# Optimization experiments

Hardware: AMD Instinct MI355X
Metric: run time of the kernel (lower is better)

The kernel has to match this reference:

```python
import jax, jax.numpy as jnp
from jax import lax
import numpy as np

N_HEAD = 16
KERNEL = 3
ROPE_BASE = 10000.0


def _rope_tables(T, D, dtype):
    inv_freq = 1.0 / (ROPE_BASE ** (jnp.arange(0, D, 2, dtype=jnp.float32) / D))
    t = jnp.arange(T, dtype=jnp.float32)
    freqs = t[:, None] * inv_freq[None, :]           # [T, D/2]
    emb = jnp.concatenate([freqs, freqs], axis=-1)   # [T, D]
    return jnp.cos(emb).astype(dtype), jnp.sin(emb).astype(dtype)


def _rotate_half(x):
    x1, x2 = jnp.split(x, 2, axis=-1)
    return jnp.concatenate([-x2, x1], axis=-1)


def setup_inputs() -> dict:
    key = jax.random.key(0)
    k1, k2, k3, k4 = jax.random.split(key, 4)
    B, T, C = 2, 2048, 2048
    s = 0.02
    return {
        "x": jax.random.normal(k1, (B, T, C), dtype=jnp.float32),
        "conv_w": jax.random.normal(k2, (C, 1, KERNEL), dtype=jnp.float32) * s,
        "w_attn": jax.random.normal(k3, (3 * C, C), dtype=jnp.float32) * s,
        "w_proj": jax.random.normal(k4, (C, C), dtype=jnp.float32) * s,
    }


def reference(x, conv_w, w_attn, w_proj):
    B, T, C = x.shape
    H = N_HEAD
    D = C // H

    # causal depthwise conv1d: left-pad K-1, groups=C
    xc = jnp.transpose(x, (0, 2, 1))                       # [B, C, T]
    xc = jnp.pad(xc, ((0, 0), (0, 0), (KERNEL - 1, 0)))
    xc = lax.conv_general_dilated(
        xc, conv_w, window_strides=(1,), padding="VALID",
        feature_group_count=C, dimension_numbers=("NCH", "OIH", "NCH"))
    xconv = jnp.transpose(xc, (0, 2, 1))                   # [B, T, C]

    # fused QKV projection
    qkv = xconv @ w_attn.T                                 # [B, T, 3C]
    q, k, v = jnp.split(qkv, 3, axis=-1)
    q = q.reshape(B, T, H, D)
    k = k.reshape(B, T, H, D)
    v = v.reshape(B, T, H, D)

    # rotary embedding
    cos, sin = _rope_tables(T, D, x.dtype)                 # [T, D]
    cos = cos[None, :, None, :]
    sin = sin[None, :, None, :]
    q = q * cos + _rotate_half(q) * sin
    k = k * cos + _rotate_half(k) * sin

    # causal SDPA
    scale = 1.0 / jnp.sqrt(jnp.asarray(D, dtype=x.dtype))
    scores = jnp.einsum("bthd,bshd->bhts", q, k) * scale   # [B, H, T, T]
    causal = jnp.tril(jnp.ones((T, T), dtype=bool))
    scores = jnp.where(causal[None, None], scores, jnp.finfo(scores.dtype).min)
    p = jax.nn.softmax(scores, axis=-1)
    y = jnp.einsum("bhts,bshd->bthd", p, v).reshape(B, T, C)

    return y @ w_proj.T
```

## Files before the change

kernel.cpp:

```cpp
#include <hip/hip_runtime.h>

typedef __attribute__((ext_vector_type(8))) short bf16x8;
typedef __attribute__((ext_vector_type(4))) float f32x4;
typedef __attribute__((ext_vector_type(4))) unsigned short u16x4;

#define DEV static __device__ __forceinline__

DEV float bf2f(unsigned short u) {
  union { unsigned int i; float f; } v; v.i = ((unsigned int)u) << 16; return v.f;
}
DEV unsigned short f2bf(float f) {
  unsigned int x = __float_as_uint(f);
  x += 0x7fffu + ((x >> 16) & 1u);
  return (unsigned short)(x >> 16);
}
DEV f32x4 mfma16(bf16x8 a, bf16x8 b, f32x4 c) {
  return __builtin_amdgcn_mfma_f32_16x16x32_bf16(a, b, c, 0, 0, 0);
}
DEV void gload_lds16(const void* g, void* l) {
  __builtin_amdgcn_global_load_lds(
      (const __attribute__((address_space(1))) unsigned int*)g,
      (__attribute__((address_space(3))) unsigned int*)l, 16, 0, 0);
}

__global__ void build_tables(float* __restrict__ ct, float* __restrict__ st) {
  int idx = blockIdx.x * 256 + threadIdx.x;
  int i = idx & 63, t = idx >> 6;
  float f = powf(10000.0f, -(float)i * (1.0f / 64.0f));
  float a = (float)t * f;
  ct[idx] = cosf(a);
  st[idx] = sinf(a);
}

__global__ void cast_bf(const float* __restrict__ in, unsigned short* __restrict__ out, int n4) {
  int idx = blockIdx.x * 256 + threadIdx.x;
  if (idx >= n4) return;
  f32x4 v = *(const f32x4*)(in + (size_t)idx * 4);
  u16x4 o;
  #pragma unroll
  for (int j = 0; j < 4; ++j) o[j] = f2bf(v[j]);
  *(u16x4*)(out + (size_t)idx * 4) = o;
}

__global__ void conv_cast(const float* __restrict__ x, const float* __restrict__ w,
                          unsigned short* __restrict__ out) {
  int idx = blockIdx.x * 256 + threadIdx.x;
  int c4 = idx & 511, t = (idx >> 9) & 2047;
  int c = c4 * 4;
  const float* xp = x + (size_t)(idx >> 20) * 2048 * 2048 + (size_t)t * 2048 + c;
  f32x4 v2 = *(const f32x4*)xp;
  f32x4 v1 = {0.f, 0.f, 0.f, 0.f}, v0 = {0.f, 0.f, 0.f, 0.f};
  if (t >= 1) v1 = *(const f32x4*)(xp - 2048);
  if (t >= 2) v0 = *(const f32x4*)(xp - 4096);
  u16x4 o;
  #pragma unroll
  for (int j = 0; j < 4; ++j) {
    float val = v0[j] * w[(c + j) * 3 + 0] + v1[j] * w[(c + j) * 3 + 1] + v2[j] * w[(c + j) * 3 + 2];
    o[j] = f2bf(val);
  }
  *(u16x4*)(idx * 4 + out) = o;
}

template <int MFRAG, int NFRAG, bool OUT_BF16>
__global__ __launch_bounds__(512, 2) void gemm2p(const unsigned short* __restrict__ A,
                                                 const unsigned short* __restrict__ Bw,
                                                 void* __restrict__ Cp, int M, int N, int K) {
  constexpr int BM = MFRAG * 32;
  constexpr int BN = NFRAG * 64;
  constexpr int ALD = BM / 128;
  constexpr int BLD = BN / 128;
  constexpr int STEADY = 2 * (ALD + BLD);
  constexpr int HALF = ALD + BLD;
  __shared__ __align__(16) unsigned short As[2][2][BM * 32];
  __shared__ __align__(16) unsigned short Bs[2][2][BN * 32];
  const int tid = threadIdx.x;
  const int w = tid >> 6, l = tid & 63;
  const int lr = l & 15, lg = l >> 4;
  const int wm = w >> 2, wn = w & 3;
  const int nbx = N / BN, nby = M / BM;
  const int nwg = nbx * nby;
  const int bid = blockIdx.x;
  const int wg = (bid & 7) * (nwg >> 3) + (bid >> 3);
  const int bx = wg / nby, by = wg % nby;
  const int m0 = by * BM, n0 = bx * BN;

  int aOff[ALD], bOff[BLD];
  #pragma unroll
  for (int it = 0; it < ALD; ++it) {
    int q = it * 512 + tid, row = q >> 2, cp = q & 3;
    aOff[it] = (m0 + row) * K + ((cp ^ ((row >> 1) & 3)) * 8);
  }
  #pragma unroll
  for (int it = 0; it < BLD; ++it) {
    int q = it * 512 + tid, row = q >> 2, cp = q & 3;
    bOff[it] = (n0 + row) * K + ((cp ^ ((row >> 1) & 3)) * 8);
  }
  const int dstW = w * 512;

  int aRd[MFRAG], bRd[NFRAG];
  #pragma unroll
  for (int m = 0; m < MFRAG; ++m) {
    int R = wm * (MFRAG * 16) + m * 16 + lr;
    aRd[m] = R * 32 + ((lg ^ ((R >> 1) & 3)) * 8);
  }
  #pragma unroll
  for (int n = 0; n < NFRAG; ++n) {
    int R = wn * (NFRAG * 16) + n * 16 + lr;
    bRd[n] = R * 32 + ((lg ^ ((R >> 1) & 3)) * 8);
  }

  auto stageA = [&](int tt, int kh) {
    const unsigned short* s = A + (size_t)(tt * 64 + kh * 32);
    unsigned short* d = (unsigned short*)As[tt & 1][kh] + dstW;
    #pragma unroll
    for (int it = 0; it < ALD; ++it) gload_lds16(s + aOff[it], d + it * 4096);
  };
  auto stageB = [&](int tt, int kh) {
    const unsigned short* s = Bw + (size_t)(tt * 64 + kh * 32);
    unsigned short* d = (unsigned short*)Bs[tt & 1][kh] + dstW;
    #pragma unroll
    for (int it = 0; it < BLD; ++it) gload_lds16(s + bOff[it], d + it * 4096);
  };
  #define WAIT_STEADY do { if constexpr (STEADY == 8) asm volatile("s_waitcnt vmcnt(8)" ::: "memory"); \
                           else asm volatile("s_waitcnt vmcnt(6)" ::: "memory"); } while (0)
  #define WAIT_HALF   do { if constexpr (HALF == 4) asm volatile("s_waitcnt vmcnt(4)" ::: "memory"); \
                           else asm volatile("s_waitcnt vmcnt(3)" ::: "memory"); } while (0)
  #define WAIT_ZERO   asm volatile("s_waitcnt vmcnt(0)" ::: "memory")

  #define PH(BUF, KH, STAGE_STMT, WAIT_STMT)                              \
  {                                                                       \
    const unsigned short* Ab = (const unsigned short*)As[BUF][KH];        \
    const unsigned short* Bb = (const unsigned short*)Bs[BUF][KH];        \
    bf16x8 aF[MFRAG], bF[NFRAG];                                          \
    _Pragma("unroll") for (int m = 0; m < MFRAG; ++m)                     \
        aF[m] = *(const bf16x8*)(Ab + aRd[m]);                            \
    _Pragma("unroll") for (int n = 0; n < NFRAG; ++n)                     \
        bF[n] = *(const bf16x8*)(Bb + bRd[n]);                            \
    STAGE_STMT;                                                           \
    __builtin_amdgcn_sched_barrier(0);                                    \
    __builtin_amdgcn_s_barrier();                                         \
    __builtin_amdgcn_sched_barrier(0);                                    \
    __builtin_amdgcn_s_setprio(1);                                        \
    _Pragma("unroll") for (int m = 0; m < MFRAG; ++m)                     \
      _Pragma("unroll") for (int n = 0; n < NFRAG; ++n)                   \
          acc[m][n] = mfma16(aF[m], bF[n], acc[m][n]);                    \
    __builtin_amdgcn_s_setprio(0);                                        \
    WAIT_STMT;                                                            \
    __builtin_amdgcn_sched_barrier(0);                                    \
    __builtin_amdgcn_s_barrier();                                         \
    __builtin_amdgcn_sched_barrier(0);                                    \
  }

  f32x4 acc[MFRAG][NFRAG] = {};
  const int NT = K >> 6;
  stageA(0, 0); stageB(0, 0);
  stageA(0, 1); stageB(0, 1);
  stageA(1, 0); stageB(1, 0);
  __builtin_amdgcn_sched_barrier(0);
  WAIT_STEADY;
  __builtin_amdgcn_s_barrier();
  __builtin_amdgcn_sched_barrier(0);

  int t = 0;
  for (; t + 2 < NT; ++t) {
    PH(t & 1, 0, { stageA(t + 1, 1); stageB(t + 1, 1); }, WAIT_STEADY);
    PH(t & 1, 1, { stageA(t + 2, 0); stageB(t + 2, 0); }, WAIT_STEADY);
  }
  PH(t & 1, 0, { stageA(t + 1, 1); stageB(t + 1, 1); }, WAIT_STEADY);
  PH(t & 1, 1, {}, WAIT_HALF);
  ++t;
  PH(t & 1, 0, {}, WAIT_ZERO);
  PH(t & 1, 1, {}, {});
  #undef PH
  #undef WAIT_STEADY
  #undef WAIT_HALF
  #undef WAIT_ZERO

  #pragma unroll
  for (int m = 0; m < MFRAG; ++m)
    #pragma unroll
    for (int r = 0; r < 4; ++r) {
      int row = m0 + wm * (MFRAG * 16) + m * 16 + lg * 4 + r;
      #pragma unroll
      for (int n = 0; n < NFRAG; ++n) {
        int col = n0 + wn * (NFRAG * 16) + n * 16 + lr;
        if (OUT_BF16) ((unsigned short*)Cp)[(size_t)row * N + col] = f2bf(acc[m][n][r]);
        else          ((float*)Cp)[(size_t)row * N + col] = acc[m][n][r];
      }
    }
}

__global__ __launch_bounds__(256) void rope_vt(const unsigned short* __restrict__ qkv,
                                               const float* __restrict__ ct,
                                               const float* __restrict__ st,
                                               unsigned short* __restrict__ Qo,
                                               unsigned short* __restrict__ Ko,
                                               unsigned short* __restrict__ Vt) {
  __shared__ unsigned short tile[64][136];
  const int bh = blockIdx.x, tt = blockIdx.y;
  const int b = bh >> 4, h = bh & 15;
  const unsigned short* base = qkv + ((size_t)(b * 2048 + tt * 64)) * 6144 + h * 128;
  {
    const int r = threadIdx.x >> 2, ch = threadIdx.x & 3;
    const unsigned short* vsrc = base + 4096 + (size_t)r * 6144;
    #pragma unroll
    for (int it = 0; it < 4; ++it) {
      int d0 = (ch * 4 + it) * 8;
      *(bf16x8*)&tile[r][d0] = *(const bf16x8*)(vsrc + d0);
    }
  }
  {
    const int i = threadIdx.x & 63, rr = threadIdx.x >> 6;
    #pragma unroll
    for (int jj = 0; jj < 16; ++jj) {
      int r = rr * 16 + jj;
      int t = tt * 64 + r;
      const unsigned short* src = base + (size_t)r * 6144;
      float cz = ct[t * 64 + i], sz = st[t * 64 + i];
      float q1 = bf2f(src[i]),        q2 = bf2f(src[i + 64]);
      float k1 = bf2f(src[2048 + i]), k2 = bf2f(src[2048 + i + 64]);
      size_t o = ((size_t)bh * 2048 + t) * 128 + i;
      Qo[o]      = f2bf(q1 * cz - q2 * sz);
      Qo[o + 64] = f2bf(q2 * cz + q1 * sz);
      Ko[o]      = f2bf(k1 * cz - k2 * sz);
      Ko[o + 64] = f2bf(k2 * cz + k1 * sz);
    }
  }
  __syncthreads();
  {
    const int d = threadIdx.x >> 1, half = threadIdx.x & 1;
    unsigned short* dst = Vt + ((size_t)bh * 128 + d) * 2048 + tt * 64;
    #pragma unroll
    for (int it = 0; it < 4; ++it) {
      int t0 = half * 32 + it * 8;
      bf16x8 v;
      #pragma unroll
      for (int j = 0; j < 8; ++j) ((unsigned short*)&v)[j] = tile[t0 + j][d];
      *(bf16x8*)(dst + t0) = v;
    }
  }
}

__global__ __launch_bounds__(256, 4) void attn_fwd(const unsigned short* __restrict__ Q,
                                                   const unsigned short* __restrict__ K,
                                                   const unsigned short* __restrict__ Vt,
                                                   unsigned short* __restrict__ Y) {
  const int T = 2048, D = 128, C = 2048;
  __shared__ __align__(16) unsigned short Ks[64 * 128];
  __shared__ __align__(16) unsigned short Vs[128 * 64];
  __shared__ __align__(16) unsigned short Pl[4][16 * 64];
  const int tid = threadIdx.x;
  const int w = tid >> 6, l = tid & 63;
  const int lr = l & 15, lg = l >> 4;
  const int bh = blockIdx.x;
  const int qi = (int)gridDim.y - 1 - (int)blockIdx.y;
  const int qbase = qi * 64;
  const size_t base = (size_t)bh * T * D;

  bf16x8 qf[4];
  {
    const unsigned short* qp = Q + base + (size_t)(qbase + w * 16 + lr) * D + lg * 8;
    #pragma unroll
    for (int d = 0; d < 4; ++d) qf[d] = *(const bf16x8*)(qp + d * 32);
  }
  int kSrc[4], vSrc[4], ldsDst[4];
  #pragma unroll
  for (int it = 0; it < 4; ++it) {
    int c = it * 256 + tid;
    int krow = c >> 4, kdc = c & 15;
    kSrc[it] = krow * D + ((kdc ^ (krow & 7)) * 8);
    int vd = c >> 3, vcc = c & 7;
    vSrc[it] = vd * T + ((vcc ^ (vd & 7)) * 8);
    ldsDst[it] = (it * 256 + w * 64) * 8;
  }
  f32x4 ao[8] = {};
  float mrun = -3.0e38f, lrun = 0.0f;
  const float cs = 0.08838834764831845f * 1.4426950408889634f;
  const int q_abs = qbase + w * 16 + lr;

  for (int kt = 0; kt <= qi; ++kt) {
    const int kv0 = kt * 64;
    #pragma unroll
    for (int it = 0; it < 4; ++it) {
      gload_lds16(K + base + (size_t)kv0 * D + kSrc[it], Ks + ldsDst[it]);
      gload_lds16(Vt + base + kv0 + vSrc[it], Vs + ldsDst[it]);
    }
    __syncthreads();
    f32x4 s4[4] = {};
    __builtin_amdgcn_s_setprio(1);
    #pragma unroll
    for (int n = 0; n < 4; ++n) {
      int row = n * 16 + lr;
      #pragma unroll
      for (int d = 0; d < 4; ++d) {
        bf16x8 kf = *(const bf16x8*)(Ks + row * 128 + (((d * 4 + lg) ^ (lr & 7)) * 8));
        s4[n] = mfma16(kf, qf[d], s4[n]);
      }
    }
    __builtin_amdgcn_s_setprio(0);
    if (kt == qi) {
      #pragma unroll
      for (int n = 0; n < 4; ++n)
        #pragma unroll
        for (int r = 0; r < 4; ++r)
          if (kv0 + n * 16 + lg * 4 + r > q_abs) s4[n][r] = -3.0e38f;
    }
    float mx = -3.0e38f;
    #pragma unroll
    for (int n = 0; n < 4; ++n)
      #pragma unroll
      for (int r = 0; r < 4; ++r) mx = fmaxf(mx, s4[n][r]);
    mx = fmaxf(mx, __shfl_xor(mx, 16, 64));
    mx = fmaxf(mx, __shfl_xor(mx, 32, 64));
    float mnew = fmaxf(mrun, mx);
    float fac = exp2f((mrun - mnew) * cs);
    mrun = mnew;
    float sum = 0.0f;
    #pragma unroll
    for (int n = 0; n < 4; ++n)
      #pragma unroll
      for (int r = 0; r < 4; ++r) {
        float p = exp2f((s4[n][r] - mnew) * cs);
        s4[n][r] = p;
        sum += p;
      }
    sum += __shfl_xor(sum, 16, 64);
    sum += __shfl_xor(sum, 32, 64);
    lrun = lrun * fac + sum;
    float fr[4];
    #pragma unroll
    for (int r = 0; r < 4; ++r) fr[r] = __shfl(fac, (l & 48) | (lg * 4 + r), 64);
    #pragma unroll
    for (int n8 = 0; n8 < 8; ++n8)
      #pragma unroll
      for (int r = 0; r < 4; ++r) ao[n8][r] *= fr[r];
    unsigned short* pw = (unsigned short*)Pl[w];
    #pragma unroll
    for (int n = 0; n < 4; ++n)
      #pragma unroll
      for (int i = 0; i < 2; ++i) {
        unsigned int pk = (unsigned int)f2bf(s4[n][2 * i]) |
                          ((unsigned int)f2bf(s4[n][2 * i + 1]) << 16);
        int kv = n * 16 + lg * 4 + 2 * i;
        *(unsigned int*)(pw + lr * 64 + (((kv >> 3) ^ (lr & 7)) * 8) + (kv & 7)) = pk;
      }
    __builtin_amdgcn_s_setprio(1);
    #pragma unroll
    for (int ks = 0; ks < 2; ++ks) {
      bf16x8 pa = *(const bf16x8*)(pw + lr * 64 + (((ks * 4 + lg) ^ (lr & 7)) * 8));
      #pragma unroll
      for (int n = 0; n < 8; ++n) {
        int row = n * 16 + lr;
        bf16x8 vb = *(const bf16x8*)(Vs + row * 64 + (((ks * 4 + lg) ^ (lr & 7)) * 8));
        ao[n] = mfma16(pa, vb, ao[n]);
      }
    }
    __builtin_amdgcn_s_setprio(0);
    __syncthreads();
  }
  const int b = bh >> 4, h = bh & 15;
  #pragma unroll
  for (int r = 0; r < 4; ++r) {
    float lsum = __shfl(lrun, (l & 48) | (lg * 4 + r), 64);
    float inv = 1.0f / lsum;
    int t = qbase + w * 16 + lg * 4 + r;
    unsigned short* dst = Y + ((size_t)b * T + t) * C + h * D;
    #pragma unroll
    for (int n = 0; n < 8; ++n) dst[n * 16 + lr] = f2bf(ao[n][r] * inv);
  }
}

extern "C" void kernel_launch(void* const* d_in, const int* in_sizes, int n_in,
                              void* d_out, int out_size, void* d_ws, size_t ws_size,
                              hipStream_t stream) {
  const float* x      = (const float*)d_in[0];
  const float* conv_w = (const float*)d_in[1];
  const float* w_attn = (const float*)d_in[2];
  const float* w_proj = (const float*)d_in[3];
  float* out = (float*)d_out;
  char* ws = (char*)d_ws;

  unsigned short* qkv  = (unsigned short*)(ws);
  unsigned short* qb   = (unsigned short*)(ws + 50331648);
  unsigned short* kb   = (unsigned short*)(ws + 67108864);
  unsigned short* vt   = (unsigned short*)(ws + 83886080);
  unsigned short* xcy  = (unsigned short*)(ws + 100663296);
  unsigned short* wbuf = (unsigned short*)(ws + 117440512);
  float* ctab = (float*)(ws + 142606336);
  float* stab = (float*)(ws + 143130624);

  build_tables<<<512, 256, 0, stream>>>(ctab, stab);
  cast_bf<<<12288, 256, 0, stream>>>(w_attn, wbuf, 3145728);
  conv_cast<<<8192, 256, 0, stream>>>(x, conv_w, xcy);
  gemm2p<8, 4, true><<<384, 512, 0, stream>>>(xcy, wbuf, (void*)qkv, 4096, 6144, 2048);
  rope_vt<<<dim3(32, 32), 256, 0, stream>>>(qkv, ctab, stab, qb, kb, vt);
  cast_bf<<<4096, 256, 0, stream>>>(w_proj, wbuf, 1048576);
  attn_fwd<<<dim3(32, 32), 256, 0, stream>>>(qb, kb, vt, xcy);
  gemm2p<4, 4, false><<<256, 512, 0, stream>>>(xcy, wbuf, (void*)out, 4096, 2048, 2048);
}
```

Before: 293.6 us.

## Double attention query tile to 128 rows so each K/V tile is reused twice

Each attention block now handles 128 query rows instead of 64, with each wave owning two 16-row query fragments that share every K and V tile loaded into LDS. The grid is halved along the query axis, which halves K/V global-to-LDS traffic and the number of barriers per unit of work. In exchange it doubles accumulator and score registers, lowers the occupancy hint from 4 to 2 blocks per CU, and does a little extra masked work on the diagonal tiles.

```diff
diff --git a/kernel.cpp b/kernel.cpp
--- a/kernel.cpp
+++ b/kernel.cpp
@@ -241,27 +241,28 @@
   }
 }
 
-__global__ __launch_bounds__(256, 4) void attn_fwd(const unsigned short* __restrict__ Q,
+__global__ __launch_bounds__(256, 2) void attn_fwd(const unsigned short* __restrict__ Q,
                                                    const unsigned short* __restrict__ K,
                                                    const unsigned short* __restrict__ Vt,
                                                    unsigned short* __restrict__ Y) {
   const int T = 2048, D = 128, C = 2048;
   __shared__ __align__(16) unsigned short Ks[64 * 128];
   __shared__ __align__(16) unsigned short Vs[128 * 64];
-  __shared__ __align__(16) unsigned short Pl[4][16 * 64];
+  __shared__ __align__(16) unsigned short Pl[4][32 * 64];
   const int tid = threadIdx.x;
   const int w = tid >> 6, l = tid & 63;
   const int lr = l & 15, lg = l >> 4;
   const int bh = blockIdx.x;
   const int qi = (int)gridDim.y - 1 - (int)blockIdx.y;
-  const int qbase = qi * 64;
+  const int qbase = qi * 128;
   const size_t base = (size_t)bh * T * D;
 
-  bf16x8 qf[4];
-  {
-    const unsigned short* qp = Q + base + (size_t)(qbase + w * 16 + lr) * D + lg * 8;
-    #pragma unroll
-    for (int d = 0; d < 4; ++d) qf[d] = *(const bf16x8*)(qp + d * 32);
+  bf16x8 qf[2][4];
+  #pragma unroll
+  for (int j = 0; j < 2; ++j) {
+    const unsigned short* qp = Q + base + (size_t)(qbase + w * 32 + j * 16 + lr) * D + lg * 8;
+    #pragma unroll
+    for (int d = 0; d < 4; ++d) qf[j][d] = *(const bf16x8*)(qp + d * 32);
   }
   int kSrc[4], vSrc[4], ldsDst[4];
   #pragma unroll
@@ -273,12 +274,15 @@
     vSrc[it] = vd * T + ((vcc ^ (vd & 7)) * 8);
     ldsDst[it] = (it * 256 + w * 64) * 8;
   }
-  f32x4 ao[8] = {};
-  float mrun = -3.0e38f, lrun = 0.0f;
+  f32x4 ao[2][8] = {};
+  float mrun[2] = {-3.0e38f, -3.0e38f}, lrun[2] = {0.0f, 0.0f};
   const float cs = 0.08838834764831845f * 1.4426950408889634f;
-  const int q_abs = qbase + w * 16 + lr;
-
-  for (int kt = 0; kt <= qi; ++kt) {
+  int q_abs[2];
+  #pragma unroll
+  for (int j = 0; j < 2; ++j) q_abs[j] = qbase + w * 32 + j * 16 + lr;
+
+  const int NKT = 2 * qi + 2;
+  for (int kt = 0; kt < NKT; ++kt) {
     const int kv0 = kt * 64;
     #pragma unroll
     for (int it = 0; it < 4; ++it) {
@@ -286,7 +290,7 @@
       gload_lds16(Vt + base + kv0 + vSrc[it], Vs + ldsDst[it]);
     }
     __syncthreads();
-    f32x4 s4[4] = {};
+    f32x4 s4[2][4] = {};
     __builtin_amdgcn_s_setprio(1);
     #pragma unroll
     for (int n = 0; n < 4; ++n) {
@@ -294,65 +298,76 @@
       #pragma unroll
       for (int d = 0; d < 4; ++d) {
         bf16x8 kf = *(const bf16x8*)(Ks + row * 128 + (((d * 4 + lg) ^ (lr & 7)) * 8));
-        s4[n] = mfma16(kf, qf[d], s4[n]);
+        s4[0][n] = mfma16(kf, qf[0][d], s4[0][n]);
+        s4[1][n] = mfma16(kf, qf[1][d], s4[1][n]);
       }
     }
     __builtin_amdgcn_s_setprio(0);
-    if (kt == qi) {
+    if (kt >= 2 * qi) {
+      #pragma unroll
+      for (int j = 0; j < 2; ++j)
+        #pragma unroll
+        for (int n = 0; n < 4; ++n)
+          #pragma unroll
+          for (int r = 0; r < 4; ++r)
+            if (kv0 + n * 16 + lg * 4 + r > q_abs[j]) s4[j][n][r] = -3.0e38f;
+    }
+    #pragma unroll
+    for (int j = 0; j < 2; ++j) {
+      float mx = -3.0e38f;
       #pragma unroll
       for (int n = 0; n < 4; ++n)
         #pragma unroll
-        for (int r = 0; r < 4; ++r)
-          if (kv0 + n * 16 + lg * 4 + r > q_abs) s4[n][r] = -3.0e38f;
-    }
-    float mx = -3.0e38f;
-    #pragma unroll
-    for (int n = 0; n < 4; ++n)
-      #pragma unroll
-      for (int r = 0; r < 4; ++r) mx = fmaxf(mx, s4[n][r]);
-    mx = fmaxf(mx, __shfl_xor(mx, 16, 64));
-    mx = fmaxf(mx, __shfl_xor(mx, 32, 64));
-    float mnew = fmaxf(mrun, mx);
-    float fac = exp2f((mrun - mnew) * cs);
-    mrun = mnew;
-    float sum = 0.0f;
-    #pragma unroll
-    for (int n = 0; n < 4; ++n)
-      #pragma unroll
-      for (int r = 0; r < 4; ++r) {
-        float p = exp2f((s4[n][r] - mnew) * cs);
-        s4[n][r] = p;
-        sum += p;
-      }
-    sum += __shfl_xor(sum, 16, 64);
-    sum += __shfl_xor(sum, 32, 64);
-    lrun = lrun * fac + sum;
-    float fr[4];
-    #pragma unroll
-    for (int r = 0; r < 4; ++r) fr[r] = __shfl(fac, (l & 48) | (lg * 4 + r), 64);
-    #pragma unroll
-    for (int n8 = 0; n8 < 8; ++n8)
-      #pragma unroll
-      for (int r = 0; r < 4; ++r) ao[n8][r] *= fr[r];
-    unsigned short* pw = (unsigned short*)Pl[w];
-    #pragma unroll
-    for (int n = 0; n < 4; ++n)
-      #pragma unroll
-      for (int i = 0; i < 2; ++i) {
-        unsigned int pk = (unsigned int)f2bf(s4[n][2 * i]) |
-                          ((unsigned int)f2bf(s4[n][2 * i + 1]) << 16);
-        int kv = n * 16 + lg * 4 + 2 * i;
-        *(unsigned int*)(pw + lr * 64 + (((kv >> 3) ^ (lr & 7)) * 8) + (kv & 7)) = pk;
-      }
+        for (int r = 0; r < 4; ++r) mx = fmaxf(mx, s4[j][n][r]);
+      mx = fmaxf(mx, __shfl_xor(mx, 16, 64));
+      mx = fmaxf(mx, __shfl_xor(mx, 32, 64));
+      float mnew = fmaxf(mrun[j], mx);
+      float fac = exp2f((mrun[j] - mnew) * cs);
+      mrun[j] = mnew;
+      float sum = 0.0f;
+      #pragma unroll
+      for (int n = 0; n < 4; ++n)
+        #pragma unroll
+        for (int r = 0; r < 4; ++r) {
+          float p = exp2f((s4[j][n][r] - mnew) * cs);
+          s4[j][n][r] = p;
+          sum += p;
+        }
+      sum += __shfl_xor(sum, 16, 64);
+      sum += __shfl_xor(sum, 32, 64);
+      lrun[j] = lrun[j] * fac + sum;
+      float fr[4];
+      #pragma unroll
+      for (int r = 0; r < 4; ++r) fr[r] = __shfl(fac, (l & 48) | (lg * 4 + r), 64);
+      #pragma unroll
+      for (int n8 = 0; n8 < 8; ++n8)
+        #pragma unroll
+        for (int r = 0; r < 4; ++r) ao[j][n8][r] *= fr[r];
+      unsigned short* pw = (unsigned short*)Pl[w];
+      #pragma unroll
+      for (int n = 0; n < 4; ++n)
+        #pragma unroll
+        for (int i = 0; i < 2; ++i) {
+          unsigned int pk = (unsigned int)f2bf(s4[j][n][2 * i]) |
+                            ((unsigned int)f2bf(s4[j][n][2 * i + 1]) << 16);
+          int kv = n * 16 + lg * 4 + 2 * i;
+          *(unsigned int*)(pw + (j * 16 + lr) * 64 + (((kv >> 3) ^ (lr & 7)) * 8) + (kv & 7)) = pk;
+        }
+    }
     __builtin_amdgcn_s_setprio(1);
-    #pragma unroll
-    for (int ks = 0; ks < 2; ++ks) {
-      bf16x8 pa = *(const bf16x8*)(pw + lr * 64 + (((ks * 4 + lg) ^ (lr & 7)) * 8));
-      #pragma unroll
-      for (int n = 0; n < 8; ++n) {
-        int row = n * 16 + lr;
-        bf16x8 vb = *(const bf16x8*)(Vs + row * 64 + (((ks * 4 + lg) ^ (lr & 7)) * 8));
-        ao[n] = mfma16(pa, vb, ao[n]);
+    {
+      unsigned short* pw = (unsigned short*)Pl[w];
+      #pragma unroll
+      for (int ks = 0; ks < 2; ++ks) {
+        bf16x8 pa0 = *(const bf16x8*)(pw + lr * 64 + (((ks * 4 + lg) ^ (lr & 7)) * 8));
+        bf16x8 pa1 = *(const bf16x8*)(pw + (16 + lr) * 64 + (((ks * 4 + lg) ^ (lr & 7)) * 8));
+        #pragma unroll
+        for (int n = 0; n < 8; ++n) {
+          int row = n * 16 + lr;
+          bf16x8 vb = *(const bf16x8*)(Vs + row * 64 + (((ks * 4 + lg) ^ (lr & 7)) * 8));
+          ao[0][n] = mfma16(pa0, vb, ao[0][n]);
+          ao[1][n] = mfma16(pa1, vb, ao[1][n]);
+        }
       }
     }
     __builtin_amdgcn_s_setprio(0);
@@ -360,14 +375,16 @@
   }
   const int b = bh >> 4, h = bh & 15;
   #pragma unroll
-  for (int r = 0; r < 4; ++r) {
-    float lsum = __shfl(lrun, (l & 48) | (lg * 4 + r), 64);
-    float inv = 1.0f / lsum;
-    int t = qbase + w * 16 + lg * 4 + r;
-    unsigned short* dst = Y + ((size_t)b * T + t) * C + h * D;
-    #pragma unroll
-    for (int n = 0; n < 8; ++n) dst[n * 16 + lr] = f2bf(ao[n][r] * inv);
-  }
+  for (int j = 0; j < 2; ++j)
+    #pragma unroll
+    for (int r = 0; r < 4; ++r) {
+      float lsum = __shfl(lrun[j], (l & 48) | (lg * 4 + r), 64);
+      float inv = 1.0f / lsum;
+      int t = qbase + w * 32 + j * 16 + lg * 4 + r;
+      unsigned short* dst = Y + ((size_t)b * T + t) * C + h * D;
+      #pragma unroll
+      for (int n = 0; n < 8; ++n) dst[n * 16 + lr] = f2bf(ao[j][n][r] * inv);
+    }
 }
 
 extern "C" void kernel_launch(void* const* d_in, const int* in_sizes, int n_in,
@@ -395,6 +412,6 @@
   gemm2p<8, 4, true><<<384, 512, 0, stream>>>(xcy, wbuf, (void*)qkv, 4096, 6144, 2048);
   rope_vt<<<dim3(32, 32), 256, 0, stream>>>(qkv, ctab, stab, qb, kb, vt);
   cast_bf<<<4096, 256, 0, stream>>>(w_proj, wbuf, 1048576);
-  attn_fwd<<<dim3(32, 32), 256, 0, stream>>>(qb, kb, vt, xcy);
+  attn_fwd<<<dim3(32, 16), 256, 0, stream>>>(qb, kb, vt, xcy);
   gemm2p<4, 4, false><<<256, 512, 0, stream>>>(xcy, wbuf, (void*)out, 4096, 2048, 2048);
 }
```

Result: slower. 306.4 us (+4.3%).
